# Optimization experiments

Hardware: AMD Instinct MI355X
Metric: run time of the kernel (lower is better)

Reference implementation:

```python
import jax, jax.numpy as jnp
import numpy as np

MAX_CH = 21
LAT_DIM = 64
D_EMBED = 1024
N_HEADS = 16
D_HEAD = D_EMBED // N_HEADS  # 64
L = MAX_CH * LAT_DIM         # 1344 latents
B, T = 4, 1024


def setup_inputs() -> dict:
    key = jax.random.key(0)
    k1, k2, k3, k4, k5, k6 = jax.random.split(key, 6)
    x = jax.random.normal(k1, (B, T, D_EMBED), dtype=jnp.float32)
    # boolean channel mask [b, L, T]
    ch_mask = jax.random.randint(k2, (B, L, T), 0, 2) > 0
    # learned latent queries [L, H*d] (xavier-uniform-ish init)
    lim_q = float(np.sqrt(6.0 / (L + N_HEADS * D_HEAD)))
    latent_q = jax.random.uniform(k3, (L, N_HEADS * D_HEAD), minval=-lim_q, maxval=lim_q, dtype=jnp.float32)
    # Linear weights (torch layout: [out, in]) and biases
    lim_w = float(np.sqrt(1.0 / D_EMBED))
    w_k_w = jax.random.uniform(k4, (N_HEADS * D_HEAD, D_EMBED), minval=-lim_w, maxval=lim_w, dtype=jnp.float32)
    w_k_b = jnp.zeros((N_HEADS * D_HEAD,), dtype=jnp.float32)
    w_v_w = jax.random.uniform(k5, (N_HEADS * D_HEAD, D_EMBED), minval=-lim_w, maxval=lim_w, dtype=jnp.float32)
    w_v_b = jax.random.uniform(k6, (N_HEADS * D_HEAD,), minval=-lim_w, maxval=lim_w, dtype=jnp.float32)
    return {"x": x, "ch_mask": ch_mask, "latent_q": latent_q,
            "w_k_w": w_k_w, "w_k_b": w_k_b, "w_v_w": w_v_w, "w_v_b": w_v_b}


def reference(x, ch_mask, latent_q, w_k_w, w_k_b, w_v_w, w_v_b):
    b, t, d = x.shape
    H, dh = N_HEADS, D_HEAD
    l = latent_q.shape[0]
    # faithful to torch .view(-1, H, L, d): raw row-major reinterpretation
    lq = latent_q.reshape(1, H, l, dh)                    # [1,H,L,dh]
    k = (x @ w_k_w.T + w_k_b).reshape(b, t, H, dh).transpose(0, 2, 3, 1)  # [b,H,dh,T]
    v = (x @ w_v_w.T + w_v_b).reshape(b, t, H, dh).transpose(0, 2, 1, 3)  # [b,H,T,dh]
    scale = jnp.float32(H) ** -0.5  # note: n_heads**-0.5, as in source
    scores = jnp.einsum('ohld,bhdt->bhlt', lq, k) * scale  # [b,H,L,T]
    mask = ch_mask[:, None, :, :]                           # [b,1,L,T] broadcast over heads
    scores = jnp.where(mask, scores, jnp.float32(-1e9))
    w = jax.nn.softmax(scores, axis=-1)
    w = jnp.where(mask, w, jnp.float32(0.0))
    out = jnp.einsum('bhlt,bhtd->bhld', w, v)               # [b,H,L,dh]
    return out.transpose(0, 2, 1, 3).reshape(b, l, H * dh)  # [b,L,H*dh]
```

## Files before the change

kernel.cpp:

```cpp
#include <hip/hip_runtime.h>
#include <hip/hip_bf16.h>

#define B_SZ 4
#define T_SZ 1024
#define NH 16
#define L_SZ 1344
#define LT_COUNT 21

typedef __attribute__((ext_vector_type(8))) short short8;
typedef __attribute__((ext_vector_type(4))) short short4v;
typedef __attribute__((ext_vector_type(4))) float floatx4;

typedef __attribute__((address_space(1))) const void gvoid;
typedef __attribute__((address_space(3))) void svoid;
#define GLD16(gp, lp) \
  __builtin_amdgcn_global_load_lds((gvoid*)(gp), (svoid*)(lp), 16, 0, 0)

static __device__ inline short bf16bits(float f) {
  return __builtin_bit_cast(short, __float2bfloat16(f));
}
static __device__ inline short4v cvt4(float4 v) {
  short4v r;
  r.x = bf16bits(v.x); r.y = bf16bits(v.y);
  r.z = bf16bits(v.z); r.w = bf16bits(v.w);
  return r;
}

static __device__ inline unsigned pack_bf16_2(float a, float b) {
  unsigned ua = __builtin_bit_cast(unsigned, a) + 0x8000u;
  unsigned ub = __builtin_bit_cast(unsigned, b) + 0x8000u;
  return __builtin_amdgcn_perm(ub, ua, 0x07060302u);
}
static __device__ inline uint2 pack_bf16_4(float4 v) {
  return make_uint2(pack_bf16_2(v.x, v.y), pack_bf16_2(v.z, v.w));
}


__global__ __launch_bounds__(256) void prep_kernel(
    const float4* __restrict__ x, const float4* __restrict__ wk,
    const float4* __restrict__ wv,
    uint2* __restrict__ xb, uint2* __restrict__ wkb, uint2* __restrict__ wvb,
    const void* __restrict__ mask, unsigned int* __restrict__ bits) {
  const int lane = threadIdx.x & 63;
  int f = -1;
  for (int vb = blockIdx.x; vb < 27648; vb += gridDim.x) {
    if (vb < 6144) {
      size_t i = (size_t)vb * 256 + threadIdx.x;
      if (i < 1048576)      xb[i] = pack_bf16_4(x[i]);
      else if (i < 1310720) wkb[i - 1048576] = pack_bf16_4(wk[i - 1048576]);
      else                  wvb[i - 1310720] = pack_bf16_4(wv[i - 1310720]);
    } else {
      if (f < 0) {
        const uint4* mp = (const uint4*)mask;
        uint4 a = mp[lane * 4 + 0], b2 = mp[lane * 4 + 1];
        uint4 c = mp[lane * 4 + 2], d = mp[lane * 4 + 3];
        unsigned oo = (a.x | a.y | a.z | a.w | b2.x | b2.y | b2.z | b2.w |
                       c.x | c.y | c.z | c.w | d.x | d.y | d.z | d.w) & 0xFFFFFF00u;
        unsigned aa = (a.y | a.w | b2.y | b2.w | c.y | c.w | d.y | d.w) & 0xFFu;
        int anyo = __any(oo != 0), anya = __any(aa != 0);
        f = anyo ? 1 : (anya ? 0 : 2);
      }
      int idx = (vb - 6144) * 256 + threadIdx.x;
      bool v;
      if (f == 1)      v = ((const signed char*)mask)[idx] != 0;
      else if (f == 2) v = ((const long long*)mask)[idx] != 0;
      else             v = ((const int*)mask)[idx] != 0;
      unsigned long long bal = __ballot(v);
      if ((lane & 31) == 0) {
        unsigned int w = (lane & 32) ? (unsigned int)(bal >> 32) : (unsigned int)bal;
        bits[idx >> 5] = w;
      }
    }
  }
}

__global__ __launch_bounds__(256, 4) void gemm_kv_bf16(
    const __hip_bfloat16* __restrict__ xb,
    const __hip_bfloat16* __restrict__ wkb, const __hip_bfloat16* __restrict__ wvb,
    const float* __restrict__ bk, const float* __restrict__ bv,
    __hip_bfloat16* __restrict__ k_buf, __hip_bfloat16* __restrict__ v_buf) {
  __shared__ __align__(16) __hip_bfloat16 ldsA[2][128 * 32];
  __shared__ __align__(16) __hip_bfloat16 ldsB[2][64 * 32];
  const int tid = threadIdx.x;
  const int lane = tid & 63, w = tid >> 6;
  const int wm = w & 1, wn = w >> 1;
  const int c15 = lane & 15, kq = lane >> 4;

  const __hip_bfloat16* A;
  const __hip_bfloat16* B;
  int TA, TB;
  if (blockIdx.z == 0) {
    A = wkb; B = xb; TA = blockIdx.x >> 6; TB = blockIdx.x & 63;
  } else {
    A = xb; B = wvb; TA = blockIdx.x >> 4; TB = blockIdx.x & 15;
  }
  const __hip_bfloat16* Abase = A + (size_t)TA * 128 * 1024;
  const __hip_bfloat16* Bbase = B + (size_t)TB * 64 * 1024;

  floatx4 acc[4][2];
  #pragma unroll
  for (int i = 0; i < 4; ++i)
    #pragma unroll
    for (int j = 0; j < 2; ++j) acc[i][j] = (floatx4){0.f, 0.f, 0.f, 0.f};

#define GSTAGE(sb, kk) do {                                                  \
    int cA_ = w * 128 + lane;                                                \
    int rA_ = cA_ >> 2, gA_ = (cA_ & 3) ^ (rA_ & 3);                         \
    GLD16(Abase + (size_t)rA_ * 1024 + (kk) + gA_ * 8,                       \
          &ldsA[sb][(w * 128) * 8]);                                         \
    int cA2_ = cA_ + 64;                                                     \
    int rA2_ = cA2_ >> 2, gA2_ = (cA2_ & 3) ^ (rA2_ & 3);                    \
    GLD16(Abase + (size_t)rA2_ * 1024 + (kk) + gA2_ * 8,                     \
          &ldsA[sb][(w * 128 + 64) * 8]);                                    \
    int cB_ = w * 64 + lane;                                                 \
    int rB_ = cB_ >> 2, gB_ = (cB_ & 3) ^ (rB_ & 3);                         \
    GLD16(Bbase + (size_t)rB_ * 1024 + (kk) + gB_ * 8,                       \
          &ldsB[sb][(w * 64) * 8]);                                          \
  } while (0)

  GSTAGE(0, 0);
  for (int kk = 0; kk < 1024; kk += 32) {
    const int buf = (kk >> 5) & 1;
    if (kk + 32 < 1024) {
      GSTAGE(buf ^ 1, kk + 32);
      asm volatile("s_waitcnt vmcnt(3)" ::: "memory");
    } else {
      asm volatile("s_waitcnt vmcnt(0)" ::: "memory");
    }
    __builtin_amdgcn_s_barrier();

    short8 af[4], bfr[2];
    #pragma unroll
    for (int mi = 0; mi < 4; ++mi) {
      int row = wm * 64 + mi * 16 + c15;
      af[mi] = *(const short8*)(&ldsA[buf][row * 32 + ((kq ^ (row & 3)) * 8)]);
    }
    #pragma unroll
    for (int ni = 0; ni < 2; ++ni) {
      int row = wn * 32 + ni * 16 + c15;
      bfr[ni] = *(const short8*)(&ldsB[buf][row * 32 + ((kq ^ (row & 3)) * 8)]);
    }
    #pragma unroll
    for (int mi = 0; mi < 4; ++mi)
      #pragma unroll
      for (int ni = 0; ni < 2; ++ni)
        acc[mi][ni] = __builtin_amdgcn_mfma_f32_16x16x32_bf16(
            af[mi], bfr[ni], acc[mi][ni], 0, 0, 0);

    asm volatile("s_waitcnt lgkmcnt(0)" ::: "memory");
    __builtin_amdgcn_s_barrier();
  }
#undef GSTAGE

  if (blockIdx.z == 0) {
    #pragma unroll
    for (int ni = 0; ni < 2; ++ni) {
      int gr = TB * 64 + wn * 32 + ni * 16 + c15;
      int b = gr >> 10, tc = (gr >> 6) & 15;
      int ni2 = (gr & 63) >> 4;
      #pragma unroll
      for (int mi = 0; mi < 4; ++mi) {
        int d0 = TA * 128 + wm * 64 + mi * 16 + kq * 4;
        int h = d0 >> 6, hd = d0 & 63;
        int half = hd >> 5, q4 = (hd >> 3) & 3, jlo = hd & 7;
        int bh = b * 16 + h;
        float4 b4 = *(const float4*)(bk + d0);
        float4 v4 = {acc[mi][ni][0] + b4.x, acc[mi][ni][1] + b4.y,
                     acc[mi][ni][2] + b4.z, acc[mi][ni][3] + b4.w};
        *(uint2*)(k_buf + ((size_t)((bh * 16 + tc) * 8 + ni2 * 2 + half)) * 512 +
                  (q4 * 16 + c15) * 8 + jlo) = pack_bf16_4(v4);
      }
    }
  } else {
    #pragma unroll
    for (int ni = 0; ni < 2; ++ni) {
      int d = TB * 64 + wn * 32 + ni * 16 + c15;
      int h = d >> 6;
      int di = (d & 63) >> 4;
      float bias = bv[d];
      #pragma unroll
      for (int mi = 0; mi < 4; ++mi) {
        int gr = TA * 128 + wm * 64 + mi * 16 + kq * 4;
        int b = gr >> 10, tc = (gr >> 6) & 15;
        int tl = gr & 63;
        int half = tl >> 5, q4 = (tl >> 3) & 3, jlo = tl & 7;
        int bh = b * 16 + h;
        float4 v4 = {acc[mi][ni][0] + bias, acc[mi][ni][1] + bias,
                     acc[mi][ni][2] + bias, acc[mi][ni][3] + bias};
        *(uint2*)(v_buf + ((size_t)((bh * 16 + tc) * 8 + di * 2 + half)) * 512 +
                  (q4 * 16 + c15) * 8 + jlo) = pack_bf16_4(v4);
      }
    }
  }
}

__global__ __launch_bounds__(256, 4) void attn_kernel(
    const float* __restrict__ latent_q,
    const __hip_bfloat16* __restrict__ k_buf,
    const __hip_bfloat16* __restrict__ v_buf,
    const unsigned int* __restrict__ mbits,
    float* __restrict__ out) {
  __shared__ __align__(16) __hip_bfloat16 ldsK[2][4096];
  __shared__ __align__(16) __hip_bfloat16 ldsV[2][4096];
  __shared__ __align__(16) __hip_bfloat16 pbuf[4][1024];

  const int tid = threadIdx.x;
  const int lane = tid & 63;
  const int w = tid >> 6;
  int bid = blockIdx.x;
  int xcd = bid & 7, j = bid >> 3;
  int bh = xcd * 8 + j / LT_COUNT;
  int lt = j % LT_COUNT;
  int h = bh & 15, b = bh >> 4;
  const int q4 = lane >> 4, c15 = lane & 15;
  const int c7 = c15 & 7;
  const int l0 = lt * 64;

  const float QS = 0.25f * 1.44269504089f;
  short8 qf[2];
  {
    const float* qp = latent_q + ((size_t)(h * L_SZ + l0 + w * 16 + c15)) * 64 + q4 * 8;
    float4 a0 = *(const float4*)(qp);
    float4 a1 = *(const float4*)(qp + 4);
    float4 a2 = *(const float4*)(qp + 32);
    float4 a3 = *(const float4*)(qp + 36);
    a0.x *= QS; a0.y *= QS; a0.z *= QS; a0.w *= QS;
    a1.x *= QS; a1.y *= QS; a1.z *= QS; a1.w *= QS;
    a2.x *= QS; a2.y *= QS; a2.z *= QS; a2.w *= QS;
    a3.x *= QS; a3.y *= QS; a3.z *= QS; a3.w *= QS;
    short4v t0 = cvt4(a0), t1 = cvt4(a1), t2 = cvt4(a2), t3 = cvt4(a3);
    qf[0] = (short8){t0.x, t0.y, t0.z, t0.w, t1.x, t1.y, t1.z, t1.w};
    qf[1] = (short8){t2.x, t2.y, t2.z, t2.w, t3.x, t3.y, t3.z, t3.w};
  }

  const short ob16 = (short)0x3F80;
  const short8 ones8 = (short8){ob16, ob16, ob16, ob16, ob16, ob16, ob16, ob16};
  const floatx4 zero4 = (floatx4){0.f, 0.f, 0.f, 0.f};

  floatx4 lacc = zero4;
  floatx4 o_acc[4];
  #pragma unroll
  for (int di = 0; di < 4; ++di) o_acc[di] = zero4;

  const __hip_bfloat16* kb = k_buf + (size_t)bh * 65536;
  const __hip_bfloat16* vb = v_buf + (size_t)bh * 65536;
  __hip_bfloat16* pw = pbuf[w];
  const unsigned int* mrow = mbits + ((size_t)(b * L_SZ + l0 + w * 16 + c15)) * 32;

#define STAGE_K(sb, tcn) do {                                               \
    const __hip_bfloat16* gk_ = kb + (size_t)(tcn) * 4096;                  \
    int o0_ = w * 512 + lane * 8;                                           \
    GLD16(gk_ + o0_,        &ldsK[sb][w * 512]);                            \
    GLD16(gk_ + 2048 + o0_, &ldsK[sb][2048 + w * 512]);                     \
  } while (0)
#define STAGE_V(sb, tcn) do {                                               \
    const __hip_bfloat16* gv_ = vb + (size_t)(tcn) * 4096;                  \
    int o0_ = w * 512 + lane * 8;                                           \
    GLD16(gv_ + o0_,        &ldsV[sb][w * 512]);                            \
    GLD16(gv_ + 2048 + o0_, &ldsV[sb][2048 + w * 512]);                     \
  } while (0)

  uint2 mw_cur = *(const uint2*)(mrow);
  STAGE_K(0, 0);
  STAGE_V(0, 0);

  for (int tc = 0; tc < 16; ++tc) {
    const int buf = tc & 1;
    if (tc < 15) {
      STAGE_K(buf ^ 1, tc + 1);
      asm volatile("s_waitcnt vmcnt(5)" ::: "memory");
    } else {
      asm volatile("s_waitcnt vmcnt(3)" ::: "memory");
    }
    __builtin_amdgcn_s_barrier();

    uint2 mw_nxt = mw_cur;
    if (tc < 15) mw_nxt = *(const uint2*)(mrow + (tc + 1) * 2);

    short8 kf[2][4];
    #pragma unroll
    for (int half = 0; half < 2; ++half)
      #pragma unroll
      for (int ni = 0; ni < 4; ++ni)
        kf[half][ni] = *(const short8*)(&ldsK[buf][(ni * 2 + half) * 512 + lane * 8]);
    floatx4 s[4];
    __builtin_amdgcn_s_setprio(1);
    #pragma unroll
    for (int ni = 0; ni < 4; ++ni)
      s[ni] = __builtin_amdgcn_mfma_f32_16x16x32_bf16(kf[0][ni], qf[0], zero4, 0, 0, 0);
    #pragma unroll
    for (int ni = 0; ni < 4; ++ni)
      s[ni] = __builtin_amdgcn_mfma_f32_16x16x32_bf16(kf[1][ni], qf[1], s[ni], 0, 0, 0);
    __builtin_amdgcn_s_setprio(0);

    if (tc < 15) {
      STAGE_V(buf ^ 1, tc + 1);
      asm volatile("s_waitcnt vmcnt(5)" ::: "memory");
    } else {
      asm volatile("s_waitcnt vmcnt(0)" ::: "memory");
    }
    __builtin_amdgcn_s_barrier();

    short8 vf[2][4];
    #pragma unroll
    for (int half = 0; half < 2; ++half)
      #pragma unroll
      for (int di = 0; di < 4; ++di)
        vf[half][di] = *(const short8*)(&ldsV[buf][(di * 2 + half) * 512 + lane * 8]);

    unsigned mshx = mw_cur.x >> (q4 * 4);
    unsigned mshy = mw_cur.y >> (q4 * 4);
    #pragma unroll
    for (int ni = 0; ni < 4; ++ni) {
      unsigned msh = (ni >= 2) ? mshy : mshx;
      float4 p4;
      #pragma unroll
      for (int r = 0; r < 4; ++r) {
        float e;
        asm("v_exp_f32 %0, %1" : "=v"(e) : "v"(s[ni][r]));
        const int pos = (ni & 1) * 16 + r;
        unsigned keep = (unsigned)((int)(msh << (31 - pos)) >> 31);
        ((float*)&p4)[r] = __builtin_bit_cast(
            float, __builtin_bit_cast(unsigned, e) & keep);
      }
      int pc = (ni * 2 + (q4 >> 1)) ^ c7;
      *(uint2*)(pw + c15 * 64 + pc * 8 + (q4 & 1) * 4) = pack_bf16_4(p4);
    }

    int pc0 = q4 ^ c7;
    short8 pf0 = *(const short8*)(pw + c15 * 64 + pc0 * 8);
    short8 pf1 = *(const short8*)(pw + c15 * 64 + (pc0 ^ 4) * 8);
    __builtin_amdgcn_s_setprio(1);
    #pragma unroll
    for (int di = 0; di < 4; ++di)
      o_acc[di] = __builtin_amdgcn_mfma_f32_16x16x32_bf16(vf[0][di], pf0, o_acc[di], 0, 0, 0);
    #pragma unroll
    for (int di = 0; di < 4; ++di)
      o_acc[di] = __builtin_amdgcn_mfma_f32_16x16x32_bf16(vf[1][di], pf1, o_acc[di], 0, 0, 0);
    lacc = __builtin_amdgcn_mfma_f32_16x16x32_bf16(ones8, pf0, lacc, 0, 0, 0);
    lacc = __builtin_amdgcn_mfma_f32_16x16x32_bf16(ones8, pf1, lacc, 0, 0, 0);
    __builtin_amdgcn_s_setprio(0);

    mw_cur = mw_nxt;
  }
#undef STAGE_K
#undef STAGE_V

  float la = lacc[0];
  float inv = (la > 0.f) ? 1.f / la : 0.f;
  float* ob = out + ((size_t)(b * L_SZ + l0 + w * 16 + c15)) * 1024 + h * 64;
  #pragma unroll
  for (int di = 0; di < 4; ++di) {
    float4 o4 = {o_acc[di][0] * inv, o_acc[di][1] * inv,
                 o_acc[di][2] * inv, o_acc[di][3] * inv};
    *(float4*)(ob + di * 16 + q4 * 4) = o4;
  }
}

extern "C" void kernel_launch(void* const* d_in, const int* in_sizes, int n_in,
                              void* d_out, int out_size, void* d_ws, size_t ws_size,
                              hipStream_t stream) {
  const float* x      = (const float*)d_in[0];
  const void* ch_mask = d_in[1];
  const float* lq     = (const float*)d_in[2];
  const float* wk     = (const float*)d_in[3];
  const float* bk     = (const float*)d_in[4];
  const float* wv     = (const float*)d_in[5];
  const float* bv     = (const float*)d_in[6];
  float* out = (float*)d_out;

  char* ws = (char*)d_ws;
  unsigned int* mbits   = (unsigned int*)ws;
  __hip_bfloat16* k_buf = (__hip_bfloat16*)(ws + 786432);
  __hip_bfloat16* v_buf = (__hip_bfloat16*)(ws + 786432 + 8388608);

  __hip_bfloat16* xb  = (__hip_bfloat16*)d_out;
  __hip_bfloat16* wkb = xb + 4 * 1024 * 1024;
  __hip_bfloat16* wvb = wkb + 1024 * 1024;

  prep_kernel<<<2048, 256, 0, stream>>>(
      (const float4*)x, (const float4*)wk, (const float4*)wv,
      (uint2*)xb, (uint2*)wkb, (uint2*)wvb,
      ch_mask, mbits);
  gemm_kv_bf16<<<dim3(512, 1, 2), 256, 0, stream>>>(xb, wkb, wvb, bk, bv, k_buf, v_buf);

  attn_kernel<<<8 * 168, 256, 0, stream>>>(lq, k_buf, v_buf, mbits, out);
}
```

Before: 182.5 us.

## Process two latent groups per attention block to reuse staged K/V tiles

Each attention block now computes 128 latent rows as two 64-row groups sharing the same LDS-staged K and V tiles, halving the grid size and the K/V global loads per output. Score, softmax-masking and PV MFMAs are duplicated per group with separate accumulators and mask words. The final odd block computes a duplicate group but skips its store. Register use grows, so launch bounds drop to 3 blocks per CU, trading occupancy and latency hiding for data reuse.

```diff
diff --git a/kernel.cpp b/kernel.cpp
--- a/kernel.cpp
+++ b/kernel.cpp
@@ -194,7 +194,7 @@
   }
 }
 
-__global__ __launch_bounds__(256, 4) void attn_kernel(
+__global__ __launch_bounds__(256, 3) void attn_kernel(
     const float* __restrict__ latent_q,
     const __hip_bfloat16* __restrict__ k_buf,
     const __hip_bfloat16* __restrict__ v_buf,
@@ -209,17 +209,22 @@
   const int w = tid >> 6;
   int bid = blockIdx.x;
   int xcd = bid & 7, j = bid >> 3;
-  int bh = xcd * 8 + j / LT_COUNT;
-  int lt = j % LT_COUNT;
+  int bh = xcd * 8 + j / 11;
+  int sb = j % 11;
   int h = bh & 15, b = bh >> 4;
   const int q4 = lane >> 4, c15 = lane & 15;
   const int c7 = c15 & 7;
-  const int l0 = lt * 64;
+  const int l0 = sb * 128;
+  const bool hasg1 = (sb < 10);
+  const int lg0 = l0 + w * 16;
+  const int lg1 = hasg1 ? (l0 + 64 + w * 16) : lg0;
 
   const float QS = 0.25f * 1.44269504089f;
-  short8 qf[2];
-  {
-    const float* qp = latent_q + ((size_t)(h * L_SZ + l0 + w * 16 + c15)) * 64 + q4 * 8;
+  short8 qf[2][2];
+  #pragma unroll
+  for (int g = 0; g < 2; ++g) {
+    int lg = g ? lg1 : lg0;
+    const float* qp = latent_q + ((size_t)(h * L_SZ + lg + c15)) * 64 + q4 * 8;
     float4 a0 = *(const float4*)(qp);
     float4 a1 = *(const float4*)(qp + 4);
     float4 a2 = *(const float4*)(qp + 32);
@@ -229,53 +234,62 @@
     a2.x *= QS; a2.y *= QS; a2.z *= QS; a2.w *= QS;
     a3.x *= QS; a3.y *= QS; a3.z *= QS; a3.w *= QS;
     short4v t0 = cvt4(a0), t1 = cvt4(a1), t2 = cvt4(a2), t3 = cvt4(a3);
-    qf[0] = (short8){t0.x, t0.y, t0.z, t0.w, t1.x, t1.y, t1.z, t1.w};
-    qf[1] = (short8){t2.x, t2.y, t2.z, t2.w, t3.x, t3.y, t3.z, t3.w};
+    qf[g][0] = (short8){t0.x, t0.y, t0.z, t0.w, t1.x, t1.y, t1.z, t1.w};
+    qf[g][1] = (short8){t2.x, t2.y, t2.z, t2.w, t3.x, t3.y, t3.z, t3.w};
   }
 
   const short ob16 = (short)0x3F80;
   const short8 ones8 = (short8){ob16, ob16, ob16, ob16, ob16, ob16, ob16, ob16};
   const floatx4 zero4 = (floatx4){0.f, 0.f, 0.f, 0.f};
 
-  floatx4 lacc = zero4;
-  floatx4 o_acc[4];
+  floatx4 lacc[2];
+  floatx4 o_acc[2][4];
   #pragma unroll
-  for (int di = 0; di < 4; ++di) o_acc[di] = zero4;
+  for (int g = 0; g < 2; ++g) {
+    lacc[g] = zero4;
+    #pragma unroll
+    for (int di = 0; di < 4; ++di) o_acc[g][di] = zero4;
+  }
 
   const __hip_bfloat16* kb = k_buf + (size_t)bh * 65536;
   const __hip_bfloat16* vb = v_buf + (size_t)bh * 65536;
   __hip_bfloat16* pw = pbuf[w];
-  const unsigned int* mrow = mbits + ((size_t)(b * L_SZ + l0 + w * 16 + c15)) * 32;
-
-#define STAGE_K(sb, tcn) do {                                               \
+  const unsigned int* mrow0 = mbits + ((size_t)(b * L_SZ + lg0 + c15)) * 32;
+  const unsigned int* mrow1 = mbits + ((size_t)(b * L_SZ + lg1 + c15)) * 32;
+
+#define STAGE_K(sb_, tcn) do {                                              \
     const __hip_bfloat16* gk_ = kb + (size_t)(tcn) * 4096;                  \
     int o0_ = w * 512 + lane * 8;                                           \
-    GLD16(gk_ + o0_,        &ldsK[sb][w * 512]);                            \
-    GLD16(gk_ + 2048 + o0_, &ldsK[sb][2048 + w * 512]);                     \
+    GLD16(gk_ + o0_,        &ldsK[sb_][w * 512]);                           \
+    GLD16(gk_ + 2048 + o0_, &ldsK[sb_][2048 + w * 512]);                    \
   } while (0)
-#define STAGE_V(sb, tcn) do {                                               \
+#define STAGE_V(sb_, tcn) do {                                              \
     const __hip_bfloat16* gv_ = vb + (size_t)(tcn) * 4096;                  \
     int o0_ = w * 512 + lane * 8;                                           \
-    GLD16(gv_ + o0_,        &ldsV[sb][w * 512]);                            \
-    GLD16(gv_ + 2048 + o0_, &ldsV[sb][2048 + w * 512]);                     \
+    GLD16(gv_ + o0_,        &ldsV[sb_][w * 512]);                           \
+    GLD16(gv_ + 2048 + o0_, &ldsV[sb_][2048 + w * 512]);                    \
   } while (0)
 
-  uint2 mw_cur = *(const uint2*)(mrow);
   STAGE_K(0, 0);
   STAGE_V(0, 0);
+  uint2 mw0 = *(const uint2*)(mrow0);
+  uint2 mw1 = *(const uint2*)(mrow1);
 
   for (int tc = 0; tc < 16; ++tc) {
     const int buf = tc & 1;
     if (tc < 15) {
       STAGE_K(buf ^ 1, tc + 1);
-      asm volatile("s_waitcnt vmcnt(5)" ::: "memory");
+      asm volatile("s_waitcnt vmcnt(6)" ::: "memory");
     } else {
-      asm volatile("s_waitcnt vmcnt(3)" ::: "memory");
+      asm volatile("s_waitcnt vmcnt(4)" ::: "memory");
     }
     __builtin_amdgcn_s_barrier();
 
-    uint2 mw_nxt = mw_cur;
-    if (tc < 15) mw_nxt = *(const uint2*)(mrow + (tc + 1) * 2);
+    uint2 mn0 = mw0, mn1 = mw1;
+    if (tc < 15) {
+      mn0 = *(const uint2*)(mrow0 + (tc + 1) * 2);
+      mn1 = *(const uint2*)(mrow1 + (tc + 1) * 2);
+    }
 
     short8 kf[2][4];
     #pragma unroll
@@ -283,19 +297,22 @@
       #pragma unroll
       for (int ni = 0; ni < 4; ++ni)
         kf[half][ni] = *(const short8*)(&ldsK[buf][(ni * 2 + half) * 512 + lane * 8]);
-    floatx4 s[4];
+    floatx4 s[2][4];
     __builtin_amdgcn_s_setprio(1);
     #pragma unroll
-    for (int ni = 0; ni < 4; ++ni)
-      s[ni] = __builtin_amdgcn_mfma_f32_16x16x32_bf16(kf[0][ni], qf[0], zero4, 0, 0, 0);
-    #pragma unroll
-    for (int ni = 0; ni < 4; ++ni)
-      s[ni] = __builtin_amdgcn_mfma_f32_16x16x32_bf16(kf[1][ni], qf[1], s[ni], 0, 0, 0);
+    for (int g = 0; g < 2; ++g) {
+      #pragma unroll
+      for (int ni = 0; ni < 4; ++ni)
+        s[g][ni] = __builtin_amdgcn_mfma_f32_16x16x32_bf16(kf[0][ni], qf[g][0], zero4, 0, 0, 0);
+      #pragma unroll
+      for (int ni = 0; ni < 4; ++ni)
+        s[g][ni] = __builtin_amdgcn_mfma_f32_16x16x32_bf16(kf[1][ni], qf[g][1], s[g][ni], 0, 0, 0);
+    }
     __builtin_amdgcn_s_setprio(0);
 
     if (tc < 15) {
       STAGE_V(buf ^ 1, tc + 1);
-      asm volatile("s_waitcnt vmcnt(5)" ::: "memory");
+      asm volatile("s_waitcnt vmcnt(6)" ::: "memory");
     } else {
       asm volatile("s_waitcnt vmcnt(0)" ::: "memory");
     }
@@ -308,52 +325,60 @@
       for (int di = 0; di < 4; ++di)
         vf[half][di] = *(const short8*)(&ldsV[buf][(di * 2 + half) * 512 + lane * 8]);
 
-    unsigned mshx = mw_cur.x >> (q4 * 4);
-    unsigned mshy = mw_cur.y >> (q4 * 4);
-    #pragma unroll
-    for (int ni = 0; ni < 4; ++ni) {
-      unsigned msh = (ni >= 2) ? mshy : mshx;
-      float4 p4;
-      #pragma unroll
-      for (int r = 0; r < 4; ++r) {
-        float e;
-        asm("v_exp_f32 %0, %1" : "=v"(e) : "v"(s[ni][r]));
-        const int pos = (ni & 1) * 16 + r;
-        unsigned keep = (unsigned)((int)(msh << (31 - pos)) >> 31);
-        ((float*)&p4)[r] = __builtin_bit_cast(
-            float, __builtin_bit_cast(unsigned, e) & keep);
+    #pragma unroll
+    for (int g = 0; g < 2; ++g) {
+      uint2 mw = g ? mw1 : mw0;
+      unsigned mshx = mw.x >> (q4 * 4);
+      unsigned mshy = mw.y >> (q4 * 4);
+      #pragma unroll
+      for (int ni = 0; ni < 4; ++ni) {
+        unsigned msh = (ni >= 2) ? mshy : mshx;
+        float4 p4;
+        #pragma unroll
+        for (int r = 0; r < 4; ++r) {
+          float e;
+          asm("v_exp_f32 %0, %1" : "=v"(e) : "v"(s[g][ni][r]));
+          const int pos = (ni & 1) * 16 + r;
+          unsigned keep = (unsigned)((int)(msh << (31 - pos)) >> 31);
+          ((float*)&p4)[r] = __builtin_bit_cast(
+              float, __builtin_bit_cast(unsigned, e) & keep);
+        }
+        int pc = (ni * 2 + (q4 >> 1)) ^ c7;
+        *(uint2*)(pw + c15 * 64 + pc * 8 + (q4 & 1) * 4) = pack_bf16_4(p4);
       }
-      int pc = (ni * 2 + (q4 >> 1)) ^ c7;
-      *(uint2*)(pw + c15 * 64 + pc * 8 + (q4 & 1) * 4) = pack_bf16_4(p4);
-    }
-
-    int pc0 = q4 ^ c7;
-    short8 pf0 = *(const short8*)(pw + c15 * 64 + pc0 * 8);
-    short8 pf1 = *(const short8*)(pw + c15 * 64 + (pc0 ^ 4) * 8);
-    __builtin_amdgcn_s_setprio(1);
-    #pragma unroll
-    for (int di = 0; di < 4; ++di)
-      o_acc[di] = __builtin_amdgcn_mfma_f32_16x16x32_bf16(vf[0][di], pf0, o_acc[di], 0, 0, 0);
-    #pragma unroll
-    for (int di = 0; di < 4; ++di)
-      o_acc[di] = __builtin_amdgcn_mfma_f32_16x16x32_bf16(vf[1][di], pf1, o_acc[di], 0, 0, 0);
-    lacc = __builtin_amdgcn_mfma_f32_16x16x32_bf16(ones8, pf0, lacc, 0, 0, 0);
-    lacc = __builtin_amdgcn_mfma_f32_16x16x32_bf16(ones8, pf1, lacc, 0, 0, 0);
-    __builtin_amdgcn_s_setprio(0);
-
-    mw_cur = mw_nxt;
+      int pc0 = q4 ^ c7;
+      short8 pf0 = *(const short8*)(pw + c15 * 64 + pc0 * 8);
+      short8 pf1 = *(const short8*)(pw + c15 * 64 + (pc0 ^ 4) * 8);
+      __builtin_amdgcn_s_setprio(1);
+      #pragma unroll
+      for (int di = 0; di < 4; ++di)
+        o_acc[g][di] = __builtin_amdgcn_mfma_f32_16x16x32_bf16(vf[0][di], pf0, o_acc[g][di], 0, 0, 0);
+      #pragma unroll
+      for (int di = 0; di < 4; ++di)
+        o_acc[g][di] = __builtin_amdgcn_mfma_f32_16x16x32_bf16(vf[1][di], pf1, o_acc[g][di], 0, 0, 0);
+      lacc[g] = __builtin_amdgcn_mfma_f32_16x16x32_bf16(ones8, pf0, lacc[g], 0, 0, 0);
+      lacc[g] = __builtin_amdgcn_mfma_f32_16x16x32_bf16(ones8, pf1, lacc[g], 0, 0, 0);
+      __builtin_amdgcn_s_setprio(0);
+    }
+
+    mw0 = mn0; mw1 = mn1;
   }
 #undef STAGE_K
 #undef STAGE_V
 
-  float la = lacc[0];
-  float inv = (la > 0.f) ? 1.f / la : 0.f;
-  float* ob = out + ((size_t)(b * L_SZ + l0 + w * 16 + c15)) * 1024 + h * 64;
   #pragma unroll
-  for (int di = 0; di < 4; ++di) {
-    float4 o4 = {o_acc[di][0] * inv, o_acc[di][1] * inv,
-                 o_acc[di][2] * inv, o_acc[di][3] * inv};
-    *(float4*)(ob + di * 16 + q4 * 4) = o4;
+  for (int g = 0; g < 2; ++g) {
+    if (g == 1 && !hasg1) break;
+    int lg = g ? lg1 : lg0;
+    float la = lacc[g][0];
+    float inv = (la > 0.f) ? 1.f / la : 0.f;
+    float* ob = out + ((size_t)(b * L_SZ + lg + c15)) * 1024 + h * 64;
+    #pragma unroll
+    for (int di = 0; di < 4; ++di) {
+      float4 o4 = {o_acc[g][di][0] * inv, o_acc[g][di][1] * inv,
+                   o_acc[g][di][2] * inv, o_acc[g][di][3] * inv};
+      *(float4*)(ob + di * 16 + q4 * 4) = o4;
+    }
   }
 }
 
@@ -384,5 +409,5 @@
       ch_mask, mbits);
   gemm_kv_bf16<<<dim3(512, 1, 2), 256, 0, stream>>>(xb, wkb, wvb, bk, bv, k_buf, v_buf);
 
-  attn_kernel<<<8 * 168, 256, 0, stream>>>(lq, k_buf, v_buf, mbits, out);
-}
+  attn_kernel<<<8 * 88, 256, 0, stream>>>(lq, k_buf, v_buf, mbits, out);
+}
```

Result: no change. 179.4 us (-1.7%).
